# Optimization experiments

Measured on AMD Instinct MI355X. Metric: run time of the kernel, lower is better.

## Reference

```python
import jax, jax.numpy as jnp
import numpy as np

N = 50000      # num nodes
E = 800000     # num edges (avg degree 16)
F_IN = 64      # num_node_features
D = 64         # layer_hidden_dim (= out_channels per layer)
H = 8          # num_heads
C = D // H     # head_dim = 8
L = 5          # num_gnn_layers


def setup_inputs() -> dict:
    key = jax.random.key(0)
    ks = jax.random.split(key, 8)
    x = jax.random.normal(ks[0], (N, F_IN), jnp.float32)
    edge_index = jax.random.randint(ks[1], (2, E), 0, N, dtype=jnp.int32)
    # input embedding Linear(F_IN, D): weight stored as [in, out]
    W_in = jax.random.normal(ks[2], (F_IN, D), jnp.float32) * 0.1
    b_in = jnp.zeros((D,), jnp.float32)
    # per-layer GAT params, stacked over L layers
    lin_w = jax.random.normal(ks[3], (L, D, D), jnp.float32) * 0.1
    lin_b = jnp.zeros((L, D), jnp.float32)
    att = jax.random.normal(ks[4], (L, H, 2 * C), jnp.float32) * 0.1
    out_bias = jnp.zeros((L, D), jnp.float32)
    ln_g = jnp.ones((L, D), jnp.float32)
    ln_b = jnp.zeros((L, D), jnp.float32)
    return {"x": x, "edge_index": edge_index, "W_in": W_in, "b_in": b_in,
            "lin_w": lin_w, "lin_b": lin_b, "att": att, "out_bias": out_bias,
            "ln_g": ln_g, "ln_b": ln_b}


def _gat_layer(h, src, dst, Wl, bl, al, ob, g, b):
    # h: [N, D] -> per-head features [N, H, C]
    hp = (h @ Wl + bl).reshape(N, H, C)
    xi = hp[dst]          # [E, H, C] target-node features (x_i)
    xj = hp[src]          # [E, H, C] source-node features (x_j)
    # cat([x_i, x_j]) . att  == x_i . att[:, :C] + x_j . att[:, C:]
    alpha = jnp.einsum('ehc,hc->eh', xi, al[:, :C]) + \
            jnp.einsum('ehc,hc->eh', xj, al[:, C:])          # [E, H]
    alpha = jax.nn.leaky_relu(alpha, negative_slope=0.2)
    # segment softmax over target index (numerically stable)
    m = jax.ops.segment_max(alpha, dst, num_segments=N)      # [N, H]
    ea = jnp.exp(alpha - m[dst])
    s = jax.ops.segment_sum(ea, dst, num_segments=N)         # [N, H]
    w = ea / (s[dst] + 1e-16)                                # [E, H]
    # message = x_j * alpha, aggr='add'
    agg = jax.ops.segment_sum(xj * w[:, :, None], dst, num_segments=N)  # [N, H, C]
    out = agg.reshape(N, H * C) + ob
    out = jax.nn.elu(out)
    # LayerNorm over feature dim (eval mode: dropout = identity)
    mu = out.mean(-1, keepdims=True)
    var = out.var(-1, keepdims=True)
    return (out - mu) * jax.lax.rsqrt(var + 1e-5) * g + b


def reference(x, edge_index, W_in, b_in, lin_w, lin_b, att, out_bias, ln_g, ln_b):
    src = edge_index[0]
    dst = edge_index[1]   # PyG source_to_target: index = edge_index[1]
    h = jax.nn.relu(x @ W_in + b_in)
    for l in range(L):
        h = _gat_layer(h, src, dst, lin_w[l], lin_b[l], att[l],
                       out_bias[l], ln_g[l], ln_b[l])
    return h
```

## Files before the change

### kernel.cpp

```cpp
#include <hip/hip_runtime.h>
#include <hip/hip_bf16.h>

#define DD 64
#define LL 5
#define KPAD 64
#define L2E 1.4426950408889634f

typedef __attribute__((ext_vector_type(8))) short short8;
typedef __attribute__((ext_vector_type(4))) float float4v;

__device__ __forceinline__ short f2bf_bits(float f) {
    __hip_bfloat16 h = __float2bfloat16(f);
    return *reinterpret_cast<short*>(&h);
}
__device__ __forceinline__ float bfbits2f(short s) {
    __hip_bfloat16 h = *reinterpret_cast<__hip_bfloat16*>(&s);
    return __bfloat162float(h);
}

__device__ __forceinline__ int sniffw(const unsigned short* xb) {
    int lane = threadIdx.x & 63;
    int e = (xb[lane * 2] >> 7) & 0xFF;
    return __any(e >= 134) ? 1 : 0;
}

__global__ void allcvt_k(const void* __restrict__ x, const void* __restrict__ W_in,
                         const void* __restrict__ b_in, const void* __restrict__ lw,
                         const void* __restrict__ lb, const void* __restrict__ att,
                         const void* __restrict__ ob, const void* __restrict__ lg,
                         const void* __restrict__ lbb,
                         unsigned short* __restrict__ xhi, unsigned short* __restrict__ xlo,
                         float* __restrict__ wts,
                         unsigned short* __restrict__ whiT, unsigned short* __restrict__ wloT,
                         int* __restrict__ deg,
                         int nelem, int nxb, int n) {
    int bid = blockIdx.x;
    int fl = sniffw((const unsigned short*)x);
    if (bid < nxb) {
        int i = bid * 256 + threadIdx.x;
        if (i < nelem) {
            float v = fl ? ((const float*)x)[i] : (float)((const __hip_bfloat16*)x)[i];
            short hi = f2bf_bits(v);
            xhi[i] = (unsigned short)hi;
            xlo[i] = (unsigned short)f2bf_bits(v - bfbits2f(hi));
        }
    } else if (bid < nxb + 104) {
        int i = (bid - nxb) * 256 + threadIdx.x;
        if (i >= 26560) return;
        const void* p; int o;
        if      (i < 4096)  { p = W_in; o = i; }
        else if (i < 4160)  { p = b_in; o = i - 4096; }
        else if (i < 24640) { p = lw;   o = i - 4160; }
        else if (i < 24960) { p = lb;   o = i - 24640; }
        else if (i < 25600) { p = att;  o = i - 24960; }
        else if (i < 25920) { p = ob;   o = i - 25600; }
        else if (i < 26240) { p = lg;   o = i - 25920; }
        else                { p = lbb;  o = i - 26240; }
        wts[i] = fl ? ((const float*)p)[o] : (float)((const __hip_bfloat16*)p)[o];
    } else if (bid < nxb + 104 + 96) {
        int i = (bid - nxb - 104) * 256 + threadIdx.x;
        if (i >= 6 * 4096) return;
        const void* p; int o;
        if (i < 4096) { p = W_in; o = i; } else { p = lw; o = i - 4096; }
        float v = fl ? ((const float*)p)[o] : (float)((const __hip_bfloat16*)p)[o];
        short hi = f2bf_bits(v);
        short lo = f2bf_bits(v - bfbits2f(hi));
        int mat = i >> 12, rem = i & 4095, k = rem >> 6, col = rem & 63;
        int t = mat * 4096 + col * 64 + k;
        whiT[t] = (unsigned short)hi;
        wloT[t] = (unsigned short)lo;
    } else {
        int i = (bid - nxb - 104 - 96) * 256 + threadIdx.x;
        if (i < n) deg[i] = 0;
    }
}

__global__ void csrpad_k(const int* __restrict__ src, const int* __restrict__ dst,
                         int* __restrict__ deg, unsigned short* __restrict__ csr_pad,
                         int e, int psize, int n) {
    int p = blockIdx.x & 7;
    int chunk = blockIdx.x >> 3;
    int lo = p * psize;
    int hi = min(lo + psize, n);
    int base = chunk * 2048 + threadIdx.x;
#pragma unroll
    for (int k = 0; k < 8; ++k) {
        int i = base + k * 256;
        if (i < e) {
            int d = dst[i];
            if (d >= lo && d < hi) {
                int slot = atomicAdd(&deg[d], 1);
                if (slot < KPAD) csr_pad[d * KPAD + slot] = (unsigned short)src[i];
            }
        }
    }
}

__device__ __forceinline__ void gemm_from_lds(
        const unsigned short (*AH)[72], const unsigned short (*AL)[72],
        const unsigned short* __restrict__ Whi, const unsigned short* __restrict__ Wlo,
        const float* __restrict__ bias, const float* __restrict__ Att,
        unsigned short* __restrict__ hp_out, float* __restrict__ bd,
        float* __restrict__ ss, int base, int n) {
    int lane = threadIdx.x & 63;
    int wave = threadIdx.x >> 6;
    int m = lane & 15;
    int q = lane >> 4;
    int coln = wave * 16 + m;

    short8 ah0 = *reinterpret_cast<const short8*>(&AH[m][q * 8]);
    short8 ah1 = *reinterpret_cast<const short8*>(&AH[m][32 + q * 8]);
    short8 al0 = *reinterpret_cast<const short8*>(&AL[m][q * 8]);
    short8 al1 = *reinterpret_cast<const short8*>(&AL[m][32 + q * 8]);

    short8 bh0 = *reinterpret_cast<const short8*>(Whi + coln * 64 + q * 8);
    short8 bh1 = *reinterpret_cast<const short8*>(Whi + coln * 64 + 32 + q * 8);
    short8 bl0 = *reinterpret_cast<const short8*>(Wlo + coln * 64 + q * 8);
    short8 bl1 = *reinterpret_cast<const short8*>(Wlo + coln * 64 + 32 + q * 8);

    float4v acc = {0.f, 0.f, 0.f, 0.f};
    acc = __builtin_amdgcn_mfma_f32_16x16x32_bf16(ah0, bh0, acc, 0, 0, 0);
    acc = __builtin_amdgcn_mfma_f32_16x16x32_bf16(al0, bh0, acc, 0, 0, 0);
    acc = __builtin_amdgcn_mfma_f32_16x16x32_bf16(ah0, bl0, acc, 0, 0, 0);
    acc = __builtin_amdgcn_mfma_f32_16x16x32_bf16(ah1, bh1, acc, 0, 0, 0);
    acc = __builtin_amdgcn_mfma_f32_16x16x32_bf16(al1, bh1, acc, 0, 0, 0);
    acc = __builtin_amdgcn_mfma_f32_16x16x32_bf16(ah1, bl1, acc, 0, 0, 0);

    float bc = bias[coln];
    int c_ = m & 7;
    int hh = 2 * wave + (m >> 3);
    float attd = Att[hh * 16 + c_];
    float atts = Att[hh * 16 + 8 + c_];
#pragma unroll
    for (int r = 0; r < 4; ++r) {
        int rr = base + q * 4 + r;
        float v = acc[r] + bc;
        short vb = f2bf_bits(v);
        float vr = bfbits2f(vb);
        if (rr < n) hp_out[(size_t)rr * 64 + coln] = (unsigned short)vb;
        float bdv = vr * attd;
        float ssv = vr * atts;
        bdv += __shfl_xor(bdv, 1, 64);
        bdv += __shfl_xor(bdv, 2, 64);
        bdv += __shfl_xor(bdv, 4, 64);
        ssv += __shfl_xor(ssv, 1, 64);
        ssv += __shfl_xor(ssv, 2, 64);
        ssv += __shfl_xor(ssv, 4, 64);
        if ((m & 7) == 0 && rr < n) {
            bd[rr * 8 + hh] = bdv * L2E;
            ss[rr * 8 + hh] = ssv * L2E;
        }
    }
}

__global__ void __launch_bounds__(256) k0_k(const unsigned short* __restrict__ xhi,
                                            const unsigned short* __restrict__ xlo,
                                            const unsigned short* __restrict__ whiT,
                                            const unsigned short* __restrict__ wloT,
                                            const float* __restrict__ bias_in,
                                            const float* __restrict__ bias_l0,
                                            const float* __restrict__ att0,
                                            unsigned short* __restrict__ hp_out,
                                            float* __restrict__ bd, float* __restrict__ ss,
                                            int n) {
    __shared__ unsigned short AH[16][72];
    __shared__ unsigned short AL[16][72];
    int lane = threadIdx.x & 63;
    int wave = threadIdx.x >> 6;
    int m = lane & 15;
    int q = lane >> 4;
    int coln = wave * 16 + m;
    int base = blockIdx.x * 16;

    {
        int arow = min(base + m, n - 1);
        const unsigned short* ap = xhi + (size_t)arow * 64 + q * 8;
        const unsigned short* alp = xlo + (size_t)arow * 64 + q * 8;
        short8 ah0 = *reinterpret_cast<const short8*>(ap);
        short8 ah1 = *reinterpret_cast<const short8*>(ap + 32);
        short8 al0 = *reinterpret_cast<const short8*>(alp);
        short8 al1 = *reinterpret_cast<const short8*>(alp + 32);
        short8 bh0 = *reinterpret_cast<const short8*>(whiT + coln * 64 + q * 8);
        short8 bh1 = *reinterpret_cast<const short8*>(whiT + coln * 64 + 32 + q * 8);
        short8 bl0 = *reinterpret_cast<const short8*>(wloT + coln * 64 + q * 8);
        short8 bl1 = *reinterpret_cast<const short8*>(wloT + coln * 64 + 32 + q * 8);
        float4v acc = {0.f, 0.f, 0.f, 0.f};
        acc = __builtin_amdgcn_mfma_f32_16x16x32_bf16(ah0, bh0, acc, 0, 0, 0);
        acc = __builtin_amdgcn_mfma_f32_16x16x32_bf16(al0, bh0, acc, 0, 0, 0);
        acc = __builtin_amdgcn_mfma_f32_16x16x32_bf16(ah0, bl0, acc, 0, 0, 0);
        acc = __builtin_amdgcn_mfma_f32_16x16x32_bf16(ah1, bh1, acc, 0, 0, 0);
        acc = __builtin_amdgcn_mfma_f32_16x16x32_bf16(al1, bh1, acc, 0, 0, 0);
        acc = __builtin_amdgcn_mfma_f32_16x16x32_bf16(ah1, bl1, acc, 0, 0, 0);
        float bc = bias_in[coln];
#pragma unroll
        for (int r = 0; r < 4; ++r) {
            float v = fmaxf(acc[r] + bc, 0.f);
            short hi = f2bf_bits(v);
            AH[q * 4 + r][coln] = (unsigned short)hi;
            AL[q * 4 + r][coln] = (unsigned short)f2bf_bits(v - bfbits2f(hi));
        }
    }
    __syncthreads();
    gemm_from_lds(AH, AL, whiT + 4096, wloT + 4096, bias_l0, att0,
                  hp_out, bd, ss, base, n);
}

__global__ void __launch_bounds__(256) layer_k(const unsigned short* __restrict__ hpbf,
                                               const int* __restrict__ deg,
                                               const unsigned short* __restrict__ csr,
                                               const float* __restrict__ bd_in,
                                               const float* __restrict__ ss_in,
                                               const float* __restrict__ ob,
                                               const float* __restrict__ g,
                                               const float* __restrict__ b,
                                               const unsigned short* __restrict__ Wnhi,
                                               const unsigned short* __restrict__ Wnlo,
                                               const float* __restrict__ bias_n,
                                               const float* __restrict__ att_n,
                                               unsigned short* __restrict__ hp_out,
                                               float* __restrict__ bd_out,
                                               float* __restrict__ ss_out,
                                               void* __restrict__ outp,
                                               const unsigned short* __restrict__ xb,
                                               int n, int last) {
    __shared__ unsigned short AH[16][72];
    __shared__ unsigned short AL[16][72];
    int lane = threadIdx.x & 63;
    int wave = threadIdx.x >> 6;
    int base = blockIdx.x * 16;

    int h1 = lane & 7;
    int e1 = lane >> 3;
    int qt = lane >> 4;
    int fq = lane & 15;
    int h2 = fq >> 1;
    int bb = qt * 32 + h2 * 4;

    int fl = last ? sniffw(xb) : 0;

    float r0 = 0.f, r1 = 0.f, r2 = 0.f, r3 = 0.f, rsum = 0.f;

    for (int nd = 0; nd < 4; ++nd) {
        int node = base + wave * 4 + nd;
        if (node < n) {
            int node_u = __builtin_amdgcn_readfirstlane(node);
            float bh1 = bd_in[node_u * 8 + h1];
            int dd = __builtin_amdgcn_readfirstlane(min(deg[node_u], KPAD));
            int nchunk = (dd + 7) >> 3;
            const unsigned short* csrn = csr + node_u * KPAD;
            const unsigned* csrd = (const unsigned*)csrn;

            float s_acc = 0.f;
            float a0 = 0.f, a1 = 0.f, a2 = 0.f, a3 = 0.f;

            int c = 0;
            for (; c + 2 <= nchunk; c += 2) {
                int slotA = c * 8 + e1;
                int slotB = slotA + 8;
                int jA1 = csrn[slotA];
                float aA = bh1 + ss_in[jA1 * 8 + h1];
                aA = (aA > 0.f) ? aA : 0.2f * aA;
                float wA = exp2f(fminf(aA, 60.f));
                float wB = 0.f;
                if (slotB < dd) {
                    int jB1 = csrn[slotB];
                    float aB = bh1 + ss_in[jB1 * 8 + h1];
                    aB = (aB > 0.f) ? aB : 0.2f * aB;
                    wB = exp2f(fminf(aB, 60.f));
                }
                s_acc += wA + wB;
                unsigned sA0 = csrd[c * 4 + 0];
                unsigned sA1 = csrd[c * 4 + 1];
                unsigned sA2 = csrd[c * 4 + 2];
                unsigned sA3 = csrd[c * 4 + 3];
                unsigned sB0 = csrd[c * 4 + 4];
                unsigned sB1 = csrd[c * 4 + 5];
                unsigned sB2 = csrd[c * 4 + 6];
                unsigned sB3 = csrd[c * 4 + 7];
#pragma unroll
                for (int p = 0; p < 2; ++p) {
                    {
                        unsigned dwlo = p ? sA2 : sA0;
                        unsigned dwhi = p ? sA3 : sA1;
                        unsigned dw = (qt & 2) ? dwhi : dwlo;
                        int j = (qt & 1) ? (int)(dw >> 16) : (int)(dw & 0xffffu);
                        j = min(j, n - 1);
                        float we = __int_as_float(
                            __builtin_amdgcn_ds_bpermute(bb + 128 * p, __float_as_int(wA)));
                        uint2 d2 = *reinterpret_cast<const uint2*>(hpbf + (size_t)j * 64 + fq * 4);
                        a0 = fmaf(__int_as_float((int)(d2.x << 16)), we, a0);
                        a1 = fmaf(__int_as_float((int)(d2.x & 0xffff0000u)), we, a1);
                        a2 = fmaf(__int_as_float((int)(d2.y << 16)), we, a2);
                        a3 = fmaf(__int_as_float((int)(d2.y & 0xffff0000u)), we, a3);
                    }
                    {
                        unsigned dwlo = p ? sB2 : sB0;
                        unsigned dwhi = p ? sB3 : sB1;
                        unsigned dw = (qt & 2) ? dwhi : dwlo;
                        int j = (qt & 1) ? (int)(dw >> 16) : (int)(dw & 0xffffu);
                        j = min(j, n - 1);
                        float we = __int_as_float(
                            __builtin_amdgcn_ds_bpermute(bb + 128 * p, __float_as_int(wB)));
                        uint2 d2 = *reinterpret_cast<const uint2*>(hpbf + (size_t)j * 64 + fq * 4);
                        a0 = fmaf(__int_as_float((int)(d2.x << 16)), we, a0);
                        a1 = fmaf(__int_as_float((int)(d2.x & 0xffff0000u)), we, a1);
                        a2 = fmaf(__int_as_float((int)(d2.y << 16)), we, a2);
                        a3 = fmaf(__int_as_float((int)(d2.y & 0xffff0000u)), we, a3);
                    }
                }
            }
            if (c < nchunk) {
                int slot = c * 8 + e1;
                float w = 0.f;
                if (slot < dd) {
                    int j1 = csrn[slot];
                    float a = bh1 + ss_in[j1 * 8 + h1];
                    a = (a > 0.f) ? a : 0.2f * a;
                    w = exp2f(fminf(a, 60.f));
                }
                s_acc += w;
                unsigned s0 = csrd[c * 4 + 0];
                unsigned s1 = csrd[c * 4 + 1];
                unsigned s2 = csrd[c * 4 + 2];
                unsigned s3 = csrd[c * 4 + 3];
#pragma unroll
                for (int p = 0; p < 2; ++p) {
                    unsigned dwlo = p ? s2 : s0;
                    unsigned dwhi = p ? s3 : s1;
                    unsigned dw = (qt & 2) ? dwhi : dwlo;
                    int j = (qt & 1) ? (int)(dw >> 16) : (int)(dw & 0xffffu);
                    j = min(j, n - 1);
                    float we = __int_as_float(
                        __builtin_amdgcn_ds_bpermute(bb + 128 * p, __float_as_int(w)));
                    uint2 d2 = *reinterpret_cast<const uint2*>(hpbf + (size_t)j * 64 + fq * 4);
                    a0 = fmaf(__int_as_float((int)(d2.x << 16)), we, a0);
                    a1 = fmaf(__int_as_float((int)(d2.x & 0xffff0000u)), we, a1);
                    a2 = fmaf(__int_as_float((int)(d2.y << 16)), we, a2);
                    a3 = fmaf(__int_as_float((int)(d2.y & 0xffff0000u)), we, a3);
                }
            }

            float ssum = s_acc;
            ssum += __shfl_xor(ssum, 8, 64);
            ssum += __shfl_xor(ssum, 16, 64);
            ssum += __shfl_xor(ssum, 32, 64);

            a0 += __shfl_xor(a0, 16, 64); a0 += __shfl_xor(a0, 32, 64);
            a1 += __shfl_xor(a1, 16, 64); a1 += __shfl_xor(a1, 32, 64);
            a2 += __shfl_xor(a2, 16, 64); a2 += __shfl_xor(a2, 32, 64);
            a3 += __shfl_xor(a3, 16, 64); a3 += __shfl_xor(a3, 32, 64);

            if (qt == nd) { r0 = a0; r1 = a1; r2 = a2; r3 = a3; rsum = ssum; }
        }
    }

    float sh = __int_as_float(
        __builtin_amdgcn_ds_bpermute((qt * 16 + h2) * 4, __float_as_int(rsum)));
    float rinv = __builtin_amdgcn_rcpf(sh + 1e-16f);
    float4 ob4 = ((const float4*)ob)[fq];
    float o0 = r0 * rinv + ob4.x;
    float o1 = r1 * rinv + ob4.y;
    float o2 = r2 * rinv + ob4.z;
    float o3 = r3 * rinv + ob4.w;
    o0 = (o0 > 0.f) ? o0 : exp2f(o0 * L2E) - 1.f;
    o1 = (o1 > 0.f) ? o1 : exp2f(o1 * L2E) - 1.f;
    o2 = (o2 > 0.f) ? o2 : exp2f(o2 * L2E) - 1.f;
    o3 = (o3 > 0.f) ? o3 : exp2f(o3 * L2E) - 1.f;

    float ps = o0 + o1 + o2 + o3;
#pragma unroll
    for (int d = 1; d < 16; d <<= 1) ps += __shfl_xor(ps, d, 64);
    float mu = ps * (1.f / 64.f);
    float d0 = o0 - mu, d1 = o1 - mu, d2v = o2 - mu, d3 = o3 - mu;
    float sq = d0 * d0 + d1 * d1 + d2v * d2v + d3 * d3;
#pragma unroll
    for (int d = 1; d < 16; d <<= 1) sq += __shfl_xor(sq, d, 64);
    float rstd = __builtin_amdgcn_rsqf(sq * (1.f / 64.f) + 1e-5f);
    float4 g4 = ((const float4*)g)[fq];
    float4 b4 = ((const float4*)b)[fq];
    float y0 = d0 * rstd * g4.x + b4.x;
    float y1 = d1 * rstd * g4.y + b4.y;
    float y2 = d2v * rstd * g4.z + b4.z;
    float y3 = d3 * rstd * g4.w + b4.w;

    int onode = base + wave * 4 + qt;
    if (!last) {
        int ridx = wave * 4 + qt;
        short hb0 = f2bf_bits(y0), hb1 = f2bf_bits(y1);
        short hb2 = f2bf_bits(y2), hb3 = f2bf_bits(y3);
        unsigned hA = (unsigned short)hb0 | ((unsigned)(unsigned short)hb1 << 16);
        unsigned hB = (unsigned short)hb2 | ((unsigned)(unsigned short)hb3 << 16);
        uint2 yh = {hA, hB};
        unsigned lA = (unsigned short)f2bf_bits(y0 - bfbits2f(hb0)) |
                      ((unsigned)(unsigned short)f2bf_bits(y1 - bfbits2f(hb1)) << 16);
        unsigned lB = (unsigned short)f2bf_bits(y2 - bfbits2f(hb2)) |
                      ((unsigned)(unsigned short)f2bf_bits(y3 - bfbits2f(hb3)) << 16);
        uint2 yl = {lA, lB};
        *reinterpret_cast<uint2*>(&AH[ridx][fq * 4]) = yh;
        *reinterpret_cast<uint2*>(&AL[ridx][fq * 4]) = yl;
    } else if (onode < n) {
        if (fl) {
            float4 y = {y0, y1, y2, y3};
            ((float4*)outp)[(size_t)onode * 16 + fq] = y;
        } else {
            unsigned lo = (unsigned short)f2bf_bits(y0) |
                          ((unsigned)(unsigned short)f2bf_bits(y1) << 16);
            unsigned hi = (unsigned short)f2bf_bits(y2) |
                          ((unsigned)(unsigned short)f2bf_bits(y3) << 16);
            uint2 y = {lo, hi};
            ((uint2*)outp)[(size_t)onode * 16 + fq] = y;
        }
    }

    if (last) return;
    __syncthreads();
    gemm_from_lds(AH, AL, Wnhi, Wnlo, bias_n, att_n, hp_out, bd_out, ss_out, base, n);
}

static void* g_pool = nullptr;
static size_t g_pool_sz = 0;

extern "C" void kernel_launch(void* const* d_in, const int* in_sizes, int n_in,
                              void* d_out, int out_size, void* d_ws, size_t ws_size,
                              hipStream_t stream) {
    const void* x    = d_in[0];
    const int* ei    = (const int*)d_in[1];
    const void* W_in = d_in[2];
    const void* b_in = d_in[3];
    const void* lw   = d_in[4];
    const void* lb   = d_in[5];
    const void* att  = d_in[6];
    const void* ob   = d_in[7];
    const void* lg   = d_in[8];
    const void* lbb  = d_in[9];

    const int n = in_sizes[0] / DD;
    const int e = in_sizes[1] / 2;
    const int* src = ei;
    const int* dst = ei + e;

    auto align256 = [](size_t v) { return (v + 255) & ~(size_t)255; };
    size_t need = 0;
    size_t off_xhi  = need; need += align256((size_t)n * DD * 2);
    size_t off_xlo  = need; need += align256((size_t)n * DD * 2);
    size_t off_hpA  = need; need += align256((size_t)n * DD * 2);
    size_t off_hpB  = need; need += align256((size_t)n * DD * 2);
    size_t off_deg  = need; need += align256((size_t)n * 4);
    size_t off_csr  = need; need += align256((size_t)n * KPAD * 2);
    size_t off_wts  = need; need += align256((size_t)26560 * 4);
    size_t off_bdA  = need; need += align256((size_t)n * 8 * 4);
    size_t off_ssA  = need; need += align256((size_t)n * 8 * 4);
    size_t off_bdB  = need; need += align256((size_t)n * 8 * 4);
    size_t off_ssB  = need; need += align256((size_t)n * 8 * 4);
    size_t off_whi  = need; need += align256((size_t)6 * 4096 * 2);
    size_t off_wlo  = need; need += align256((size_t)6 * 4096 * 2);

    char* ws;
    if (ws_size >= need) {
        ws = (char*)d_ws;
    } else {
        if (g_pool == nullptr || g_pool_sz < need) {
            hipMalloc(&g_pool, need);
            g_pool_sz = need;
        }
        ws = (char*)g_pool;
    }

    unsigned short* xhi = (unsigned short*)(ws + off_xhi);
    unsigned short* xlo = (unsigned short*)(ws + off_xlo);
    unsigned short* hpA = (unsigned short*)(ws + off_hpA);
    unsigned short* hpB = (unsigned short*)(ws + off_hpB);
    int* deg     = (int*)(ws + off_deg);
    unsigned short* csr = (unsigned short*)(ws + off_csr);
    float* wts   = (float*)(ws + off_wts);
    float* bdA   = (float*)(ws + off_bdA);
    float* ssA   = (float*)(ws + off_ssA);
    float* bdB   = (float*)(ws + off_bdB);
    float* ssB   = (float*)(ws + off_ssB);
    unsigned short* whiT = (unsigned short*)(ws + off_whi);
    unsigned short* wloT = (unsigned short*)(ws + off_wlo);

    float* wb_in = wts + 4096;
    float* wlb   = wts + 24640;
    float* watt  = wts + 24960;
    float* wob   = wts + 25600;
    float* wlg   = wts + 25920;
    float* wlbb  = wts + 26240;

    int nelem = n * DD;
    int nxb = (nelem + 255) / 256;
    int degb = (n + 255) / 256;
    allcvt_k<<<nxb + 104 + 96 + degb, 256, 0, stream>>>(
        x, W_in, b_in, lw, lb, att, ob, lg, lbb,
        xhi, xlo, wts, whiT, wloT, deg, nelem, nxb, n);

    int psize = (n + 7) / 8;
    int chunks = (e + 2047) / 2048;
    csrpad_k<<<chunks * 8, 256, 0, stream>>>(src, dst, deg, csr, e, psize, n);

    int nb16 = (n + 15) / 16;
    k0_k<<<nb16, 256, 0, stream>>>(xhi, xlo, whiT, wloT, wb_in, wlb, watt,
                                   hpA, bdA, ssA, n);

    for (int l = 0; l < LL; ++l) {
        int last = (l == LL - 1) ? 1 : 0;
        unsigned short* hin = (l & 1) ? hpB : hpA;
        float* bdi = (l & 1) ? bdB : bdA;
        float* ssi = (l & 1) ? ssB : ssA;
        unsigned short* hout = (l & 1) ? hpA : hpB;
        float* bdo = (l & 1) ? bdA : bdB;
        float* sso = (l & 1) ? ssA : ssB;
        layer_k<<<nb16, 256, 0, stream>>>(
            hin, deg, csr, bdi, ssi,
            wob + (size_t)l * DD, wlg + (size_t)l * DD, wlbb + (size_t)l * DD,
            whiT + (size_t)(l + 2) * 4096, wloT + (size_t)(l + 2) * 4096,
            wlb + (size_t)(l + 1) * DD, watt + (size_t)(l + 1) * 128,
            hout, bdo, sso, d_out, (const unsigned short*)x, n, last);
    }
}
```

Baseline: 318.7 us.

## Interleave two destination nodes per wave loop to raise gather memory parallelism

Restructures the per-wave aggregation so two target nodes are processed together in one chunk loop, issuing four independent feature gathers per iteration instead of one or two. Degrees and destination biases for the four nodes are loaded up front with a single vector load. Softmax neighbor indices now come from the already-loaded CSR dwords rather than separate per-slot loads. The aim is more memory-level parallelism and less latency exposure, at the cost of more registers and wasted work when the two nodes have unequal degrees.

```diff
diff --git a/kernel.cpp b/kernel.cpp
--- a/kernel.cpp
+++ b/kernel.cpp
@@ -238,120 +238,122 @@
 
     int fl = last ? sniffw(xb) : 0;
 
+    int nd0 = base + wave * 4;
+    int4 dv = *reinterpret_cast<const int4*>(deg + nd0);
+    int dd0 = (nd0 + 0 < n) ? min(dv.x, KPAD) : 0;
+    int dd1 = (nd0 + 1 < n) ? min(dv.y, KPAD) : 0;
+    int dd2 = (nd0 + 2 < n) ? min(dv.z, KPAD) : 0;
+    int dd3 = (nd0 + 3 < n) ? min(dv.w, KPAD) : 0;
+    float bhv0 = bd_in[min(nd0 + 0, n - 1) * 8 + h1];
+    float bhv1 = bd_in[min(nd0 + 1, n - 1) * 8 + h1];
+    float bhv2 = bd_in[min(nd0 + 2, n - 1) * 8 + h1];
+    float bhv3 = bd_in[min(nd0 + 3, n - 1) * 8 + h1];
+
     float r0 = 0.f, r1 = 0.f, r2 = 0.f, r3 = 0.f, rsum = 0.f;
 
-    for (int nd = 0; nd < 4; ++nd) {
-        int node = base + wave * 4 + nd;
-        if (node < n) {
-            int node_u = __builtin_amdgcn_readfirstlane(node);
-            float bh1 = bd_in[node_u * 8 + h1];
-            int dd = __builtin_amdgcn_readfirstlane(min(deg[node_u], KPAD));
-            int nchunk = (dd + 7) >> 3;
-            const unsigned short* csrn = csr + node_u * KPAD;
-            const unsigned* csrd = (const unsigned*)csrn;
-
-            float s_acc = 0.f;
-            float a0 = 0.f, a1 = 0.f, a2 = 0.f, a3 = 0.f;
-
-            int c = 0;
-            for (; c + 2 <= nchunk; c += 2) {
-                int slotA = c * 8 + e1;
-                int slotB = slotA + 8;
-                int jA1 = csrn[slotA];
-                float aA = bh1 + ss_in[jA1 * 8 + h1];
-                aA = (aA > 0.f) ? aA : 0.2f * aA;
-                float wA = exp2f(fminf(aA, 60.f));
-                float wB = 0.f;
-                if (slotB < dd) {
-                    int jB1 = csrn[slotB];
-                    float aB = bh1 + ss_in[jB1 * 8 + h1];
-                    aB = (aB > 0.f) ? aB : 0.2f * aB;
-                    wB = exp2f(fminf(aB, 60.f));
-                }
-                s_acc += wA + wB;
-                unsigned sA0 = csrd[c * 4 + 0];
-                unsigned sA1 = csrd[c * 4 + 1];
-                unsigned sA2 = csrd[c * 4 + 2];
-                unsigned sA3 = csrd[c * 4 + 3];
-                unsigned sB0 = csrd[c * 4 + 4];
-                unsigned sB1 = csrd[c * 4 + 5];
-                unsigned sB2 = csrd[c * 4 + 6];
-                unsigned sB3 = csrd[c * 4 + 7];
 #pragma unroll
-                for (int p = 0; p < 2; ++p) {
-                    {
-                        unsigned dwlo = p ? sA2 : sA0;
-                        unsigned dwhi = p ? sA3 : sA1;
-                        unsigned dw = (qt & 2) ? dwhi : dwlo;
-                        int j = (qt & 1) ? (int)(dw >> 16) : (int)(dw & 0xffffu);
-                        j = min(j, n - 1);
-                        float we = __int_as_float(
-                            __builtin_amdgcn_ds_bpermute(bb + 128 * p, __float_as_int(wA)));
-                        uint2 d2 = *reinterpret_cast<const uint2*>(hpbf + (size_t)j * 64 + fq * 4);
-                        a0 = fmaf(__int_as_float((int)(d2.x << 16)), we, a0);
-                        a1 = fmaf(__int_as_float((int)(d2.x & 0xffff0000u)), we, a1);
-                        a2 = fmaf(__int_as_float((int)(d2.y << 16)), we, a2);
-                        a3 = fmaf(__int_as_float((int)(d2.y & 0xffff0000u)), we, a3);
-                    }
-                    {
-                        unsigned dwlo = p ? sB2 : sB0;
-                        unsigned dwhi = p ? sB3 : sB1;
-                        unsigned dw = (qt & 2) ? dwhi : dwlo;
-                        int j = (qt & 1) ? (int)(dw >> 16) : (int)(dw & 0xffffu);
-                        j = min(j, n - 1);
-                        float we = __int_as_float(
-                            __builtin_amdgcn_ds_bpermute(bb + 128 * p, __float_as_int(wB)));
-                        uint2 d2 = *reinterpret_cast<const uint2*>(hpbf + (size_t)j * 64 + fq * 4);
-                        a0 = fmaf(__int_as_float((int)(d2.x << 16)), we, a0);
-                        a1 = fmaf(__int_as_float((int)(d2.x & 0xffff0000u)), we, a1);
-                        a2 = fmaf(__int_as_float((int)(d2.y << 16)), we, a2);
-                        a3 = fmaf(__int_as_float((int)(d2.y & 0xffff0000u)), we, a3);
-                    }
-                }
-            }
-            if (c < nchunk) {
-                int slot = c * 8 + e1;
-                float w = 0.f;
-                if (slot < dd) {
-                    int j1 = csrn[slot];
-                    float a = bh1 + ss_in[j1 * 8 + h1];
-                    a = (a > 0.f) ? a : 0.2f * a;
-                    w = exp2f(fminf(a, 60.f));
-                }
-                s_acc += w;
-                unsigned s0 = csrd[c * 4 + 0];
-                unsigned s1 = csrd[c * 4 + 1];
-                unsigned s2 = csrd[c * 4 + 2];
-                unsigned s3 = csrd[c * 4 + 3];
-#pragma unroll
-                for (int p = 0; p < 2; ++p) {
-                    unsigned dwlo = p ? s2 : s0;
-                    unsigned dwhi = p ? s3 : s1;
-                    unsigned dw = (qt & 2) ? dwhi : dwlo;
-                    int j = (qt & 1) ? (int)(dw >> 16) : (int)(dw & 0xffffu);
-                    j = min(j, n - 1);
-                    float we = __int_as_float(
-                        __builtin_amdgcn_ds_bpermute(bb + 128 * p, __float_as_int(w)));
-                    uint2 d2 = *reinterpret_cast<const uint2*>(hpbf + (size_t)j * 64 + fq * 4);
-                    a0 = fmaf(__int_as_float((int)(d2.x << 16)), we, a0);
-                    a1 = fmaf(__int_as_float((int)(d2.x & 0xffff0000u)), we, a1);
-                    a2 = fmaf(__int_as_float((int)(d2.y << 16)), we, a2);
-                    a3 = fmaf(__int_as_float((int)(d2.y & 0xffff0000u)), we, a3);
-                }
-            }
-
-            float ssum = s_acc;
-            ssum += __shfl_xor(ssum, 8, 64);
-            ssum += __shfl_xor(ssum, 16, 64);
-            ssum += __shfl_xor(ssum, 32, 64);
-
-            a0 += __shfl_xor(a0, 16, 64); a0 += __shfl_xor(a0, 32, 64);
-            a1 += __shfl_xor(a1, 16, 64); a1 += __shfl_xor(a1, 32, 64);
-            a2 += __shfl_xor(a2, 16, 64); a2 += __shfl_xor(a2, 32, 64);
-            a3 += __shfl_xor(a3, 16, 64); a3 += __shfl_xor(a3, 32, 64);
-
-            if (qt == nd) { r0 = a0; r1 = a1; r2 = a2; r3 = a3; rsum = ssum; }
-        }
+    for (int half = 0; half < 2; ++half) {
+        int ddA = half ? dd2 : dd0;
+        int ddB = half ? dd3 : dd1;
+        float bhA = half ? bhv2 : bhv0;
+        float bhB = half ? bhv3 : bhv1;
+        int uA = __builtin_amdgcn_readfirstlane(min(nd0 + half * 2, n - 1));
+        int uB = __builtin_amdgcn_readfirstlane(min(nd0 + half * 2 + 1, n - 1));
+        const unsigned* cdA = (const unsigned*)(csr + (size_t)uA * KPAD);
+        const unsigned* cdB = (const unsigned*)(csr + (size_t)uB * KPAD);
+        int ncA = (ddA + 7) >> 3;
+        int ncB = (ddB + 7) >> 3;
+        int ncm = max(ncA, ncB);
+
+        float sA = 0.f, sB = 0.f;
+        float aA0 = 0.f, aA1 = 0.f, aA2 = 0.f, aA3 = 0.f;
+        float aB0 = 0.f, aB1 = 0.f, aB2 = 0.f, aB3 = 0.f;
+
+        for (int c = 0; c < ncm; ++c) {
+            unsigned A0 = cdA[c * 4 + 0], A1 = cdA[c * 4 + 1],
+                     A2 = cdA[c * 4 + 2], A3 = cdA[c * 4 + 3];
+            unsigned B0 = cdB[c * 4 + 0], B1 = cdB[c * 4 + 1],
+                     B2 = cdB[c * 4 + 2], B3 = cdB[c * 4 + 3];
+
+            unsigned dA0 = (qt & 2) ? A1 : A0;
+            unsigned dA1 = (qt & 2) ? A3 : A2;
+            unsigned dB0 = (qt & 2) ? B1 : B0;
+            unsigned dB1 = (qt & 2) ? B3 : B2;
+            int gA0 = (qt & 1) ? (int)(dA0 >> 16) : (int)(dA0 & 0xffffu);
+            int gA1 = (qt & 1) ? (int)(dA1 >> 16) : (int)(dA1 & 0xffffu);
+            int gB0 = (qt & 1) ? (int)(dB0 >> 16) : (int)(dB0 & 0xffffu);
+            int gB1 = (qt & 1) ? (int)(dB1 >> 16) : (int)(dB1 & 0xffffu);
+            gA0 = min(gA0, n - 1); gA1 = min(gA1, n - 1);
+            gB0 = min(gB0, n - 1); gB1 = min(gB1, n - 1);
+            uint2 vA0 = *reinterpret_cast<const uint2*>(hpbf + (size_t)gA0 * 64 + fq * 4);
+            uint2 vA1 = *reinterpret_cast<const uint2*>(hpbf + (size_t)gA1 * 64 + fq * 4);
+            uint2 vB0 = *reinterpret_cast<const uint2*>(hpbf + (size_t)gB0 * 64 + fq * 4);
+            uint2 vB1 = *reinterpret_cast<const uint2*>(hpbf + (size_t)gB1 * 64 + fq * 4);
+
+            unsigned wsA = (e1 & 4) ? ((e1 & 2) ? A3 : A2) : ((e1 & 2) ? A1 : A0);
+            unsigned wsB = (e1 & 4) ? ((e1 & 2) ? B3 : B2) : ((e1 & 2) ? B1 : B0);
+            int jA = (e1 & 1) ? (int)(wsA >> 16) : (int)(wsA & 0xffffu);
+            int jB = (e1 & 1) ? (int)(wsB >> 16) : (int)(wsB & 0xffffu);
+            jA = min(jA, n - 1);
+            jB = min(jB, n - 1);
+            int slot = c * 8 + e1;
+
+            float aav = bhA + ss_in[jA * 8 + h1];
+            float abv = bhB + ss_in[jB * 8 + h1];
+            aav = (aav > 0.f) ? aav : 0.2f * aav;
+            abv = (abv > 0.f) ? abv : 0.2f * abv;
+            float wgA = (slot < ddA) ? exp2f(fminf(aav, 60.f)) : 0.f;
+            float wgB = (slot < ddB) ? exp2f(fminf(abv, 60.f)) : 0.f;
+            sA += wgA;
+            sB += wgB;
+
+            float weA0 = __int_as_float(
+                __builtin_amdgcn_ds_bpermute(bb, __float_as_int(wgA)));
+            float weA1 = __int_as_float(
+                __builtin_amdgcn_ds_bpermute(bb + 128, __float_as_int(wgA)));
+            float weB0 = __int_as_float(
+                __builtin_amdgcn_ds_bpermute(bb, __float_as_int(wgB)));
+            float weB1 = __int_as_float(
+                __builtin_amdgcn_ds_bpermute(bb + 128, __float_as_int(wgB)));
+
+            aA0 = fmaf(__int_as_float((int)(vA0.x << 16)), weA0, aA0);
+            aA1 = fmaf(__int_as_float((int)(vA0.x & 0xffff0000u)), weA0, aA1);
+            aA2 = fmaf(__int_as_float((int)(vA0.y << 16)), weA0, aA2);
+            aA3 = fmaf(__int_as_float((int)(vA0.y & 0xffff0000u)), weA0, aA3);
+            aA0 = fmaf(__int_as_float((int)(vA1.x << 16)), weA1, aA0);
+            aA1 = fmaf(__int_as_float((int)(vA1.x & 0xffff0000u)), weA1, aA1);
+            aA2 = fmaf(__int_as_float((int)(vA1.y << 16)), weA1, aA2);
+            aA3 = fmaf(__int_as_float((int)(vA1.y & 0xffff0000u)), weA1, aA3);
+            aB0 = fmaf(__int_as_float((int)(vB0.x << 16)), weB0, aB0);
+            aB1 = fmaf(__int_as_float((int)(vB0.x & 0xffff0000u)), weB0, aB1);
+            aB2 = fmaf(__int_as_float((int)(vB0.y << 16)), weB0, aB2);
+            aB3 = fmaf(__int_as_float((int)(vB0.y & 0xffff0000u)), weB0, aB3);
+            aB0 = fmaf(__int_as_float((int)(vB1.x << 16)), weB1, aB0);
+            aB1 = fmaf(__int_as_float((int)(vB1.x & 0xffff0000u)), weB1, aB1);
+            aB2 = fmaf(__int_as_float((int)(vB1.y << 16)), weB1, aB2);
+            aB3 = fmaf(__int_as_float((int)(vB1.y & 0xffff0000u)), weB1, aB3);
+        }
+
+        float ssA = sA;
+        ssA += __shfl_xor(ssA, 8, 64);
+        ssA += __shfl_xor(ssA, 16, 64);
+        ssA += __shfl_xor(ssA, 32, 64);
+        float ssB = sB;
+        ssB += __shfl_xor(ssB, 8, 64);
+        ssB += __shfl_xor(ssB, 16, 64);
+        ssB += __shfl_xor(ssB, 32, 64);
+
+        aA0 += __shfl_xor(aA0, 16, 64); aA0 += __shfl_xor(aA0, 32, 64);
+        aA1 += __shfl_xor(aA1, 16, 64); aA1 += __shfl_xor(aA1, 32, 64);
+        aA2 += __shfl_xor(aA2, 16, 64); aA2 += __shfl_xor(aA2, 32, 64);
+        aA3 += __shfl_xor(aA3, 16, 64); aA3 += __shfl_xor(aA3, 32, 64);
+        aB0 += __shfl_xor(aB0, 16, 64); aB0 += __shfl_xor(aB0, 32, 64);
+        aB1 += __shfl_xor(aB1, 16, 64); aB1 += __shfl_xor(aB1, 32, 64);
+        aB2 += __shfl_xor(aB2, 16, 64); aB2 += __shfl_xor(aB2, 32, 64);
+        aB3 += __shfl_xor(aB3, 16, 64); aB3 += __shfl_xor(aB3, 32, 64);
+
+        if (qt == half * 2)     { r0 = aA0; r1 = aA1; r2 = aA2; r3 = aA3; rsum = ssA; }
+        if (qt == half * 2 + 1) { r0 = aB0; r1 = aB1; r2 = aB2; r3 = aB3; rsum = ssB; }
     }
 
     float sh = __int_as_float(
@@ -383,7 +385,7 @@
     float y2 = d2v * rstd * g4.z + b4.z;
     float y3 = d3 * rstd * g4.w + b4.w;
 
-    int onode = base + wave * 4 + qt;
+    int onode = nd0 + qt;
     if (!last) {
         int ridx = wave * 4 + qt;
         short hb0 = f2bf_bits(y0), hb1 = f2bf_bits(y1);
```

Result: faster. 301.2 us (-5.5%).
